# Kernel optimization log

Measured on AMD Instinct MI355X. Metric: run time of the kernel, lower is better.

## Reference

```python
import jax, jax.numpy as jnp
import numpy as np

SPATIAL_SHAPES = ((64, 64), (32, 32), (16, 16), (8, 8))  # (H_l, W_l) per level
N_HEADS, N_LEVELS, N_POINTS = 8, 4, 4
EMBED, HEAD_DIM = 256, 32


def _bilinear_sample(v_lvl, loc, H, W):
    """grid_sample(mode=bilinear, padding=zeros, align_corners=False).

    v_lvl: (B, nH, H*W, d)   loc: (B, Nq, nH, P, 2) with (x, y) in [0, 1].
    Returns (B, nH, Nq, P, d).
    """
    B, nH, _, d = v_lvl.shape
    Nq, P = loc.shape[1], loc.shape[3]
    g = 2.0 * loc - 1.0                      # normalized [-1, 1]
    px = ((g[..., 0] + 1.0) * W - 1.0) * 0.5  # pixel coords, align_corners=False
    py = ((g[..., 1] + 1.0) * H - 1.0) * 0.5
    x0 = jnp.floor(px); y0 = jnp.floor(py)
    wx = px - x0; wy = py - y0
    x0i = x0.astype(jnp.int32); y0i = y0.astype(jnp.int32)
    acc = jnp.zeros((B, nH, Nq * P, d), v_lvl.dtype)
    corners = ((0, 0, (1 - wx) * (1 - wy)), (1, 0, wx * (1 - wy)),
               (0, 1, (1 - wx) * wy), (1, 1, wx * wy))
    for dx, dy, w in corners:
        xi = x0i + dx; yi = y0i + dy
        valid = (xi >= 0) & (xi < W) & (yi >= 0) & (yi < H)
        idx = jnp.clip(yi, 0, H - 1) * W + jnp.clip(xi, 0, W - 1)  # (B,Nq,nH,P)
        idx_t = idx.transpose(0, 2, 1, 3).reshape(B, nH, Nq * P)
        wm = jnp.where(valid, w, 0.0).astype(v_lvl.dtype)
        wm = wm.transpose(0, 2, 1, 3).reshape(B, nH, Nq * P, 1)
        gathered = jnp.take_along_axis(v_lvl, idx_t[..., None], axis=2)
        acc = acc + wm * gathered
    return acc.reshape(B, nH, Nq, P, d)


def setup_inputs() -> dict:
    key = jax.random.key(0)
    ks = jax.random.split(key, 12)
    B, Nq = 4, sum(H * W for H, W in SPATIAL_SHAPES)
    Nv = Nq
    s = 1.0 / np.sqrt(EMBED)
    return {
        "query": jax.random.normal(ks[0], (B, Nq, EMBED), jnp.float32),
        "value": jax.random.normal(ks[1], (B, Nv, EMBED), jnp.float32),
        "reference_points": jax.random.uniform(ks[2], (B, Nq, N_LEVELS, 2), jnp.float32),
        "value_proj_w": jax.random.normal(ks[3], (EMBED, EMBED), jnp.float32) * s,
        "value_proj_b": jnp.zeros((EMBED,), jnp.float32),
        "offsets_w": jax.random.normal(ks[4], (EMBED, N_HEADS * N_LEVELS * N_POINTS * 2), jnp.float32) * (0.05 * s),
        "offsets_b": jax.random.normal(ks[5], (N_HEADS * N_LEVELS * N_POINTS * 2,), jnp.float32) * 2.0,
        "attn_w_w": jax.random.normal(ks[6], (EMBED, N_HEADS * N_LEVELS * N_POINTS), jnp.float32) * s,
        "attn_w_b": jnp.zeros((N_HEADS * N_LEVELS * N_POINTS,), jnp.float32),
        "out_w": jax.random.normal(ks[7], (EMBED, EMBED), jnp.float32) * s,
        "out_b": jnp.zeros((EMBED,), jnp.float32),
    }


def reference(query, value, reference_points, value_proj_w, value_proj_b,
              offsets_w, offsets_b, attn_w_w, attn_w_b, out_w, out_b):
    B, Nq, C = query.shape
    Nv = value.shape[1]
    v = (value @ value_proj_w + value_proj_b).reshape(B, Nv, N_HEADS, HEAD_DIM)
    off = (query @ offsets_w + offsets_b).reshape(B, Nq, N_HEADS, N_LEVELS, N_POINTS, 2)
    aw = (query @ attn_w_w + attn_w_b).reshape(B, Nq, N_HEADS, N_LEVELS * N_POINTS)
    aw = jax.nn.softmax(aw, axis=-1).reshape(B, Nq, N_HEADS, N_LEVELS, N_POINTS)
    norm = jnp.array([[W, H] for H, W in SPATIAL_SHAPES], dtype=query.dtype)  # (L,2) as (W,H)
    loc = reference_points[:, :, None, :, None, :] + off / norm[None, None, None, :, None, :]
    out = jnp.zeros((B, Nq, N_HEADS, HEAD_DIM), query.dtype)
    cursor = 0
    for l, (H, W) in enumerate(SPATIAL_SHAPES):
        v_lvl = v[:, cursor:cursor + H * W].transpose(0, 2, 1, 3)  # (B,nH,HW,d)
        cursor += H * W
        sampled = _bilinear_sample(v_lvl, loc[:, :, :, l], H, W)   # (B,nH,Nq,P,d)
        out = out + jnp.einsum('bnhp,bhnpd->bnhd', aw[:, :, :, l], sampled)
    return out.reshape(B, Nq, C) @ out_w + out_b
```

## Files before the change

### kernel.cpp

```cpp
#include <hip/hip_runtime.h>
#include <hip/hip_bf16.h>
#include <math.h>

#define B_ 4
#define NQ 5440
#define M_ROWS (B_ * NQ)
#define NH 8
#define NL 4
#define NP 4
#define HD 32

typedef __attribute__((ext_vector_type(8))) short bf16x8;
typedef __attribute__((ext_vector_type(4))) short bf16x4;
typedef __attribute__((ext_vector_type(4))) float f32x4;
typedef _Float16 f16;

static __device__ __forceinline__ unsigned short f2bf(float f) {
  union { float f; unsigned u; } v; v.f = f;
  unsigned r = (v.u + 0x7fffu + ((v.u >> 16) & 1u)) >> 16;
  return (unsigned short)r;
}
static __device__ __forceinline__ float bits2f(unsigned u) {
  union { unsigned u; float f; } v; v.u = u; return v.f;
}

__global__ __launch_bounds__(256) void prep_all(
    const float* __restrict__ value, const float* __restrict__ query,
    unsigned short* __restrict__ value_bf, unsigned short* __restrict__ query_bf,
    const float* __restrict__ vpw, const float* __restrict__ offw,
    const float* __restrict__ attnw, const float* __restrict__ outw,
    const float* __restrict__ offb, const float* __restrict__ attnb,
    unsigned short* __restrict__ vp_t, unsigned short* __restrict__ q_t,
    unsigned short* __restrict__ out_t, float* __restrict__ biasq, int n4) {
  int id = blockIdx.x * 256 + threadIdx.x;
  if (id < 2 * n4) {
    const float* src; unsigned short* dst; int j;
    if (id < n4) { src = value; dst = value_bf; j = id; }
    else { src = query; dst = query_bf; j = id - n4; }
    float4 f = ((const float4*)src)[j];
    bf16x4 o;
    o[0] = (short)f2bf(f.x); o[1] = (short)f2bf(f.y);
    o[2] = (short)f2bf(f.z); o[3] = (short)f2bf(f.w);
    ((bf16x4*)dst)[j] = o;
    return;
  }
  int w = id - 2 * n4;
  if (w < 65536) {
    int n = w >> 8, k = w & 255;
    vp_t[w] = f2bf(vpw[k * 256 + n]);
  } else if (w < 163840) {
    int q = w - 65536; int n = q >> 8, k = q & 255;
    q_t[q] = f2bf(n < 256 ? offw[k * 256 + n] : attnw[k * 128 + (n - 256)]);
  } else if (w < 229376) {
    int o = w - 163840; int n = o >> 8, k = o & 255;
    out_t[o] = f2bf(outw[k * 256 + n]);
  } else if (w < 229760) {
    int j = w - 229376;
    biasq[j] = j < 256 ? offb[j] : attnb[j - 256];
  }
}

__global__ __launch_bounds__(256) void gemm12_kernel(
    const unsigned short* __restrict__ valbf, const unsigned short* __restrict__ qrybf,
    const unsigned short* __restrict__ wt_vp, const unsigned short* __restrict__ wt_q,
    const float* __restrict__ vp_b, const float* __restrict__ biasq,
    unsigned short* __restrict__ v_bf, f16* __restrict__ offaw_h) {
  __shared__ unsigned short Bs[8 * 64 * 32];
  const int t = threadIdx.x;
  const int lane = t & 63, wid = t >> 6;
  const int qd = lane >> 4, l16 = lane & 15;
  const int g = blockIdx.x;
  const int grp = g / 80, r = g % 80;
  int by, bx;
  if (grp < 21) { by = grp * 8 + (r & 7); bx = r >> 3; }
  else          { by = 168 + (r & 1);     bx = r >> 1; }
  const int bm = by * 128;
  const bool isv = bx < 4;
  const int bn = isv ? bx * 64 : (bx - 4) * 64;
  const unsigned short* A  = isv ? valbf : qrybf;
  const unsigned short* Wt = isv ? wt_vp : wt_q;

  const unsigned short* bg = Wt + (size_t)(bn + (t >> 2)) * 256 + (t & 3) * 8;
  unsigned short* bs_b = Bs + (t & 192) * 8;
#pragma unroll
  for (int j = 0; j < 8; ++j)
    __builtin_amdgcn_global_load_lds(
        (const __attribute__((address_space(1))) void*)(bg + j * 32),
        (__attribute__((address_space(3))) void*)(bs_b + j * 2048), 16, 0, 0);

  const unsigned short* ar0 = A + (size_t)(bm + wid * 32 + l16) * 256 + qd * 8;
  const unsigned short* ar1 = ar0 + 16 * 256;
  bf16x8 a0[8], a1[8];
#pragma unroll
  for (int j = 0; j < 8; ++j) {
    a0[j] = *(const bf16x8*)(ar0 + j * 32);
    a1[j] = *(const bf16x8*)(ar1 + j * 32);
  }
  __syncthreads();

  f32x4 acc[2][4] = {};
#pragma unroll
  for (int j = 0; j < 8; ++j) {
    const unsigned short* bt = Bs + j * 2048 + l16 * 32 + qd * 8;
#pragma unroll
    for (int ni = 0; ni < 4; ++ni) {
      const bf16x8 bf = *(const bf16x8*)(bt + ni * 512);
      acc[0][ni] = __builtin_amdgcn_mfma_f32_16x16x32_bf16(a0[j], bf, acc[0][ni], 0, 0, 0);
      acc[1][ni] = __builtin_amdgcn_mfma_f32_16x16x32_bf16(a1[j], bf, acc[1][ni], 0, 0, 0);
    }
  }
  if (isv) {
#pragma unroll
    for (int ni = 0; ni < 4; ++ni) {
      const int c = bn + ni * 16 + l16;
      const float bb = vp_b[c];
      const int h = c >> 5, d = c & 31;
#pragma unroll
      for (int mi = 0; mi < 2; ++mi)
#pragma unroll
        for (int rr = 0; rr < 4; ++rr) {
          const int gm = bm + wid * 32 + mi * 16 + qd * 4 + rr;
          const int b = gm / NQ, pix = gm - b * NQ;
          v_bf[((size_t)(b * NH + h) * NQ + pix) * HD + d] = f2bf(acc[mi][ni][rr] + bb);
        }
    }
  } else {
#pragma unroll
    for (int ni = 0; ni < 4; ++ni) {
      const int c = bn + ni * 16 + l16;
      const float bb = biasq[c];
#pragma unroll
      for (int mi = 0; mi < 2; ++mi)
#pragma unroll
        for (int rr = 0; rr < 4; ++rr) {
          const int gm = bm + wid * 32 + mi * 16 + qd * 4 + rr;
          offaw_h[(size_t)gm * 384 + c] = (f16)(acc[mi][ni][rr] + bb);
        }
    }
  }
}

__global__ __launch_bounds__(256) void gemm_out_kernel(
    const unsigned short* __restrict__ attn_bf, const unsigned short* __restrict__ wt_out,
    const float* __restrict__ out_b, float* __restrict__ out) {
  __shared__ unsigned short Bs[8 * 64 * 32];
  const int t = threadIdx.x;
  const int lane = t & 63, wid = t >> 6;
  const int qd = lane >> 4, l16 = lane & 15;
  const int g = blockIdx.x;
  const int grp = g / 32, r = g % 32;
  int by, bx;
  if (grp < 21) { by = grp * 8 + (r & 7); bx = r >> 3; }
  else          { by = 168 + (r & 1);     bx = r >> 1; }
  const int bm = by * 128, bn = bx * 64;

  const unsigned short* bg = wt_out + (size_t)(bn + (t >> 2)) * 256 + (t & 3) * 8;
  unsigned short* bs_b = Bs + (t & 192) * 8;
#pragma unroll
  for (int j = 0; j < 8; ++j)
    __builtin_amdgcn_global_load_lds(
        (const __attribute__((address_space(1))) void*)(bg + j * 32),
        (__attribute__((address_space(3))) void*)(bs_b + j * 2048), 16, 0, 0);

  const unsigned short* ar0 = attn_bf + (size_t)(bm + wid * 32 + l16) * 256 + qd * 8;
  const unsigned short* ar1 = ar0 + 16 * 256;
  bf16x8 a0[8], a1[8];
#pragma unroll
  for (int j = 0; j < 8; ++j) {
    a0[j] = *(const bf16x8*)(ar0 + j * 32);
    a1[j] = *(const bf16x8*)(ar1 + j * 32);
  }
  __syncthreads();

  f32x4 acc[2][4] = {};
#pragma unroll
  for (int j = 0; j < 8; ++j) {
    const unsigned short* bt = Bs + j * 2048 + l16 * 32 + qd * 8;
#pragma unroll
    for (int ni = 0; ni < 4; ++ni) {
      const bf16x8 bf = *(const bf16x8*)(bt + ni * 512);
      acc[0][ni] = __builtin_amdgcn_mfma_f32_16x16x32_bf16(a0[j], bf, acc[0][ni], 0, 0, 0);
      acc[1][ni] = __builtin_amdgcn_mfma_f32_16x16x32_bf16(a1[j], bf, acc[1][ni], 0, 0, 0);
    }
  }
#pragma unroll
  for (int ni = 0; ni < 4; ++ni) {
    const int c = bn + ni * 16 + l16;
    const float bb = out_b[c];
#pragma unroll
    for (int mi = 0; mi < 2; ++mi)
#pragma unroll
      for (int rr = 0; rr < 4; ++rr) {
        const int gm = bm + wid * 32 + mi * 16 + qd * 4 + rr;
        out[(size_t)gm * 256 + c] = acc[mi][ni][rr] + bb;
      }
  }
}

__global__ __launch_bounds__(256) void sample_fused_kernel(
    const unsigned short* __restrict__ v, const float* __restrict__ refp,
    const f16* __restrict__ offaw_h, unsigned short* __restrict__ out) {
  __shared__ float s_off[8 * 384];
  __shared__ float s_ref[64];
  __shared__ unsigned s_offs[16 * 64 * 4];
  __shared__ float s_wts[16 * 64 * 4];
  const int t = threadIdx.x;
  const int blk = blockIdx.x;
  const int b = (blk & 7) >> 1;
  const int q0loc = ((blk >> 3) * 2 + (blk & 1)) * 8;
  const int q0 = b * NQ + q0loc;

  {
    const unsigned* src = (const unsigned*)(offaw_h + (size_t)q0 * 384);
#pragma unroll
    for (int i = 0; i < 6; ++i) {
      const int idx = t + i * 256;
      union { unsigned u; f16 h[2]; } cv; cv.u = src[idx];
      s_off[2 * idx]     = (float)cv.h[0];
      s_off[2 * idx + 1] = (float)cv.h[1];
    }
    if (t < 64) s_ref[t] = refp[(size_t)q0 * 8 + t];
  }
  __syncthreads();
  if (t < 64) {
    float* p = s_off + (t >> 3) * 384 + 256 + (t & 7) * 16;
    float m = -1e30f;
#pragma unroll
    for (int j = 0; j < 16; ++j) m = fmaxf(m, p[j]);
    float e[16]; float s = 0.f;
#pragma unroll
    for (int j = 0; j < 16; ++j) { e[j] = __expf(p[j] - m); s += e[j]; }
    const float inv = 1.f / s;
#pragma unroll
    for (int j = 0; j < 16; ++j) p[j] = e[j] * inv;
  }
  __syncthreads();
  {
    const int qh = t & 63, q = qh >> 3, h = qh & 7, l = t >> 6;
    const int HS[NL]      = {64, 32, 16, 8};
    const int LVL_OFF[NL] = {0, 4096, 5120, 5376};
    const int H = HS[l], W = HS[l];
    const float rx = s_ref[q * 8 + l * 2 + 0];
    const float ry = s_ref[q * 8 + l * 2 + 1];
    const unsigned vbase = (unsigned)(((b * NH + h) * NQ + LVL_OFF[l]) * 64);
#pragma unroll
    for (int pp = 0; pp < 4; ++pp) {
      const int p = l * 4 + pp;
      const float ox = s_off[q * 384 + h * 32 + l * 8 + pp * 2 + 0];
      const float oy = s_off[q * 384 + h * 32 + l * 8 + pp * 2 + 1];
      const float a  = s_off[q * 384 + 256 + h * 16 + p];
      const float px = rx * (float)W + ox - 0.5f;
      const float py = ry * (float)H + oy - 0.5f;
      const float x0f = floorf(px), y0f = floorf(py);
      const int x0 = (int)x0f, y0 = (int)y0f;
      const int x1 = x0 + 1, y1 = y0 + 1;
      const float wx = px - x0f, wy = py - y0f;
      const float m_x0 = (x0 >= 0 && x0 < W) ? 1.f : 0.f;
      const float m_x1 = (x1 >= 0 && x1 < W) ? 1.f : 0.f;
      const float m_y0 = (y0 >= 0 && y0 < H) ? 1.f : 0.f;
      const float m_y1 = (y1 >= 0 && y1 < H) ? 1.f : 0.f;
      const int cx0 = min(max(x0, 0), W - 1), cx1 = min(max(x1, 0), W - 1);
      const int cy0 = min(max(y0, 0), H - 1), cy1 = min(max(y1, 0), H - 1);
      const int ti = (p * 64 + qh) * 4;
      uint4 o4;
      o4.x = vbase + (unsigned)((cy0 * W + cx0) * 64);
      o4.y = vbase + (unsigned)((cy0 * W + cx1) * 64);
      o4.z = vbase + (unsigned)((cy1 * W + cx0) * 64);
      o4.w = vbase + (unsigned)((cy1 * W + cx1) * 64);
      float4 w4;
      w4.x = a * (1.f - wx) * (1.f - wy) * m_x0 * m_y0;
      w4.y = a * wx * (1.f - wy) * m_x1 * m_y0;
      w4.z = a * (1.f - wx) * wy * m_x0 * m_y1;
      w4.w = a * wx * wy * m_x1 * m_y1;
      *(uint4*)&s_offs[ti] = o4;
      *(float4*)&s_wts[ti] = w4;
    }
  }
  __syncthreads();
  const int lane = t & 63, wave = t >> 6;
  const int qloc = wave * 2 + (lane >> 5);
  const int h = (lane >> 2) & 7, d8 = lane & 3;
  const int tqh = qloc * 8 + h;
  const char* vB = (const char*)v;
  const int dof = d8 * 16;
  float acc[8] = {};
#pragma unroll 4
  for (int p = 0; p < 16; ++p) {
    const uint4  o4 = *(const uint4*)&s_offs[(p * 64 + tqh) * 4];
    const float4 w4 = *(const float4*)&s_wts[(p * 64 + tqh) * 4];
    const unsigned off[4] = {o4.x, o4.y, o4.z, o4.w};
    const float wt[4] = {w4.x, w4.y, w4.z, w4.w};
#pragma unroll
    for (int c = 0; c < 4; ++c) {
      union { bf16x8 v8; unsigned u[4]; } cc;
      cc.v8 = *(const bf16x8*)(vB + off[c] + dof);
      const float w = wt[c];
#pragma unroll
      for (int k = 0; k < 4; ++k) {
        acc[2 * k]     += w * bits2f(cc.u[k] << 16);
        acc[2 * k + 1] += w * bits2f(cc.u[k] & 0xffff0000u);
      }
    }
  }
  const int bq = q0 + qloc;
  bf16x8 ov;
#pragma unroll
  for (int k = 0; k < 8; ++k) ov[k] = (short)f2bf(acc[k]);
  *(bf16x8*)(out + (size_t)bq * 256 + h * HD + d8 * 8) = ov;
}

extern "C" void kernel_launch(void* const* d_in, const int* in_sizes, int n_in,
                              void* d_out, int out_size, void* d_ws, size_t ws_size,
                              hipStream_t stream) {
  const float* query        = (const float*)d_in[0];
  const float* value        = (const float*)d_in[1];
  const float* refp         = (const float*)d_in[2];
  const float* value_proj_w = (const float*)d_in[3];
  const float* value_proj_b = (const float*)d_in[4];
  const float* offsets_w    = (const float*)d_in[5];
  const float* offsets_b    = (const float*)d_in[6];
  const float* attn_w_w     = (const float*)d_in[7];
  const float* attn_w_b     = (const float*)d_in[8];
  const float* out_w        = (const float*)d_in[9];
  const float* out_b        = (const float*)d_in[10];
  float* out = (float*)d_out;

  const int M = M_ROWS;
  const size_t SZ_V   = (size_t)M * 256 * 2;
  const size_t SZ_OFF = (size_t)M * 384 * 2;
  char* w = (char*)d_ws;
  unsigned short* value_bf = (unsigned short*)w;
  unsigned short* attn_bf  = (unsigned short*)w;
  unsigned short* query_bf = (unsigned short*)(w + SZ_V);
  unsigned short* v_bf     = (unsigned short*)(w + 2 * SZ_V);
  f16* offaw_h             = (f16*)(w + 3 * SZ_V);
  char* wts                = w + 3 * SZ_V + SZ_OFF;
  unsigned short* wt_vp    = (unsigned short*)wts;
  unsigned short* wt_q     = wt_vp + 65536;
  unsigned short* wt_out   = wt_q + 98304;
  float* biasq             = (float*)(wt_out + 65536);

  dim3 blk(256);
  const int n4 = M * 64;
  const int prep_blocks = (2 * n4 + 229760 + 255) / 256;
  prep_all<<<prep_blocks, blk, 0, stream>>>(
      value, query, value_bf, query_bf,
      value_proj_w, offsets_w, attn_w_w, out_w, offsets_b, attn_w_b,
      wt_vp, wt_q, wt_out, biasq, n4);
  gemm12_kernel<<<1700, blk, 0, stream>>>(
      value_bf, query_bf, wt_vp, wt_q, value_proj_b, biasq, v_bf, offaw_h);
  sample_fused_kernel<<<M / 8, blk, 0, stream>>>(v_bf, refp, offaw_h, attn_bf);
  gemm_out_kernel<<<680, blk, 0, stream>>>(attn_bf, wt_out, out_b, out);
}
```

Before: 173.7 us.

## Compute sampling weights directly from global loads with wave-shuffle softmax

The fused sampling kernel no longer stages the fp16 offsets, logits and reference points through shared memory. Each thread loads its own slice straight from global memory and computes the per-head softmax with xor-shuffles across four lanes, which removes two barriers and a serial softmax stage run by only 64 threads. Corner indices are now stored as 16-bit values, roughly halving the shared-memory index table, and the gather loop is fully unrolled per level with constant level offsets. The cost is more scattered small global loads and some extra address arithmetic in the gather loop.

```diff
diff --git a/kernel.cpp b/kernel.cpp
--- a/kernel.cpp
+++ b/kernel.cpp
@@ -200,10 +200,8 @@
 __global__ __launch_bounds__(256) void sample_fused_kernel(
     const unsigned short* __restrict__ v, const float* __restrict__ refp,
     const f16* __restrict__ offaw_h, unsigned short* __restrict__ out) {
-  __shared__ float s_off[8 * 384];
-  __shared__ float s_ref[64];
-  __shared__ unsigned s_offs[16 * 64 * 4];
-  __shared__ float s_wts[16 * 64 * 4];
+  __shared__ __align__(16) unsigned short s_idx[16 * 64 * 4];
+  __shared__ __align__(16) float s_wts[16 * 64 * 4];
   const int t = threadIdx.x;
   const int blk = blockIdx.x;
   const int b = (blk & 7) >> 1;
@@ -211,68 +209,63 @@
   const int q0 = b * NQ + q0loc;
 
   {
-    const unsigned* src = (const unsigned*)(offaw_h + (size_t)q0 * 384);
-#pragma unroll
-    for (int i = 0; i < 6; ++i) {
-      const int idx = t + i * 256;
-      union { unsigned u; f16 h[2]; } cv; cv.u = src[idx];
-      s_off[2 * idx]     = (float)cv.h[0];
-      s_off[2 * idx + 1] = (float)cv.h[1];
-    }
-    if (t < 64) s_ref[t] = refp[(size_t)q0 * 8 + t];
-  }
-  __syncthreads();
-  if (t < 64) {
-    float* p = s_off + (t >> 3) * 384 + 256 + (t & 7) * 16;
-    float m = -1e30f;
-#pragma unroll
-    for (int j = 0; j < 16; ++j) m = fmaxf(m, p[j]);
-    float e[16]; float s = 0.f;
-#pragma unroll
-    for (int j = 0; j < 16; ++j) { e[j] = __expf(p[j] - m); s += e[j]; }
+    const int lane = t & 63, wave = t >> 6;
+    const int qh = wave * 16 + (lane >> 2);
+    const int l = lane & 3;
+    const int q = qh >> 3, h = qh & 7;
+    const f16* row = offaw_h + (size_t)(q0 + q) * 384;
+    union { uint4 u4; f16 hh[8]; } off8;
+    off8.u4 = *(const uint4*)(row + h * 32 + l * 8);
+    union { uint2 u2; f16 hh[4]; } lg4;
+    lg4.u2 = *(const uint2*)(row + 256 + h * 16 + l * 4);
+    const float2 rxy = *(const float2*)(refp + (size_t)(q0 + q) * 8 + l * 2);
+
+    float lgf[4];
+#pragma unroll
+    for (int j = 0; j < 4; ++j) lgf[j] = (float)lg4.hh[j];
+    float m = fmaxf(fmaxf(lgf[0], lgf[1]), fmaxf(lgf[2], lgf[3]));
+    m = fmaxf(m, __shfl_xor(m, 1));
+    m = fmaxf(m, __shfl_xor(m, 2));
+    float e[4], s = 0.f;
+#pragma unroll
+    for (int j = 0; j < 4; ++j) { e[j] = __expf(lgf[j] - m); s += e[j]; }
+    s += __shfl_xor(s, 1);
+    s += __shfl_xor(s, 2);
     const float inv = 1.f / s;
-#pragma unroll
-    for (int j = 0; j < 16; ++j) p[j] = e[j] * inv;
-  }
-  __syncthreads();
-  {
-    const int qh = t & 63, q = qh >> 3, h = qh & 7, l = t >> 6;
-    const int HS[NL]      = {64, 32, 16, 8};
-    const int LVL_OFF[NL] = {0, 4096, 5120, 5376};
-    const int H = HS[l], W = HS[l];
-    const float rx = s_ref[q * 8 + l * 2 + 0];
-    const float ry = s_ref[q * 8 + l * 2 + 1];
-    const unsigned vbase = (unsigned)(((b * NH + h) * NQ + LVL_OFF[l]) * 64);
+
+    const int Wl = 64 >> l, Hl = 64 >> l;
+    const float pxb = rxy.x * (float)Wl - 0.5f;
+    const float pyb = rxy.y * (float)Hl - 0.5f;
 #pragma unroll
     for (int pp = 0; pp < 4; ++pp) {
       const int p = l * 4 + pp;
-      const float ox = s_off[q * 384 + h * 32 + l * 8 + pp * 2 + 0];
-      const float oy = s_off[q * 384 + h * 32 + l * 8 + pp * 2 + 1];
-      const float a  = s_off[q * 384 + 256 + h * 16 + p];
-      const float px = rx * (float)W + ox - 0.5f;
-      const float py = ry * (float)H + oy - 0.5f;
+      const float ox = (float)off8.hh[pp * 2];
+      const float oy = (float)off8.hh[pp * 2 + 1];
+      const float a  = e[pp] * inv;
+      const float px = pxb + ox;
+      const float py = pyb + oy;
       const float x0f = floorf(px), y0f = floorf(py);
       const int x0 = (int)x0f, y0 = (int)y0f;
       const int x1 = x0 + 1, y1 = y0 + 1;
       const float wx = px - x0f, wy = py - y0f;
-      const float m_x0 = (x0 >= 0 && x0 < W) ? 1.f : 0.f;
-      const float m_x1 = (x1 >= 0 && x1 < W) ? 1.f : 0.f;
-      const float m_y0 = (y0 >= 0 && y0 < H) ? 1.f : 0.f;
-      const float m_y1 = (y1 >= 0 && y1 < H) ? 1.f : 0.f;
-      const int cx0 = min(max(x0, 0), W - 1), cx1 = min(max(x1, 0), W - 1);
-      const int cy0 = min(max(y0, 0), H - 1), cy1 = min(max(y1, 0), H - 1);
+      const float m_x0 = (x0 >= 0 && x0 < Wl) ? 1.f : 0.f;
+      const float m_x1 = (x1 >= 0 && x1 < Wl) ? 1.f : 0.f;
+      const float m_y0 = (y0 >= 0 && y0 < Hl) ? 1.f : 0.f;
+      const float m_y1 = (y1 >= 0 && y1 < Hl) ? 1.f : 0.f;
+      const int cx0 = min(max(x0, 0), Wl - 1), cx1 = min(max(x1, 0), Wl - 1);
+      const int cy0 = min(max(y0, 0), Hl - 1), cy1 = min(max(y1, 0), Hl - 1);
       const int ti = (p * 64 + qh) * 4;
-      uint4 o4;
-      o4.x = vbase + (unsigned)((cy0 * W + cx0) * 64);
-      o4.y = vbase + (unsigned)((cy0 * W + cx1) * 64);
-      o4.z = vbase + (unsigned)((cy1 * W + cx0) * 64);
-      o4.w = vbase + (unsigned)((cy1 * W + cx1) * 64);
+      ushort4 i4;
+      i4.x = (unsigned short)(cy0 * Wl + cx0);
+      i4.y = (unsigned short)(cy0 * Wl + cx1);
+      i4.z = (unsigned short)(cy1 * Wl + cx0);
+      i4.w = (unsigned short)(cy1 * Wl + cx1);
       float4 w4;
       w4.x = a * (1.f - wx) * (1.f - wy) * m_x0 * m_y0;
       w4.y = a * wx * (1.f - wy) * m_x1 * m_y0;
       w4.z = a * (1.f - wx) * wy * m_x0 * m_y1;
       w4.w = a * wx * wy * m_x1 * m_y1;
-      *(uint4*)&s_offs[ti] = o4;
+      *(ushort4*)&s_idx[ti] = i4;
       *(float4*)&s_wts[ti] = w4;
     }
   }
@@ -282,23 +275,31 @@
   const int h = (lane >> 2) & 7, d8 = lane & 3;
   const int tqh = qloc * 8 + h;
   const char* vB = (const char*)v;
-  const int dof = d8 * 16;
+  const unsigned hbase = (unsigned)((b * NH + h) * NQ) * 64u + (unsigned)(d8 * 16);
   float acc[8] = {};
-#pragma unroll 4
-  for (int p = 0; p < 16; ++p) {
-    const uint4  o4 = *(const uint4*)&s_offs[(p * 64 + tqh) * 4];
-    const float4 w4 = *(const float4*)&s_wts[(p * 64 + tqh) * 4];
-    const unsigned off[4] = {o4.x, o4.y, o4.z, o4.w};
-    const float wt[4] = {w4.x, w4.y, w4.z, w4.w};
-#pragma unroll
-    for (int c = 0; c < 4; ++c) {
-      union { bf16x8 v8; unsigned u[4]; } cc;
-      cc.v8 = *(const bf16x8*)(vB + off[c] + dof);
-      const float w = wt[c];
-#pragma unroll
-      for (int k = 0; k < 4; ++k) {
-        acc[2 * k]     += w * bits2f(cc.u[k] << 16);
-        acc[2 * k + 1] += w * bits2f(cc.u[k] & 0xffff0000u);
+#pragma unroll
+  for (int l = 0; l < 4; ++l) {
+    const int LVL_OFF = (l == 0) ? 0 : (l == 1) ? 4096 : (l == 2) ? 5120 : 5376;
+    const unsigned base = hbase + (unsigned)(LVL_OFF * 64);
+#pragma unroll
+    for (int pp = 0; pp < 4; ++pp) {
+      const int p = l * 4 + pp;
+      const ushort4 i4 = *(const ushort4*)&s_idx[(p * 64 + tqh) * 4];
+      const float4 w4 = *(const float4*)&s_wts[(p * 64 + tqh) * 4];
+      const unsigned off[4] = {
+          base + ((unsigned)i4.x << 6), base + ((unsigned)i4.y << 6),
+          base + ((unsigned)i4.z << 6), base + ((unsigned)i4.w << 6)};
+      const float wt[4] = {w4.x, w4.y, w4.z, w4.w};
+#pragma unroll
+      for (int c = 0; c < 4; ++c) {
+        union { bf16x8 v8; unsigned u[4]; } cc;
+        cc.v8 = *(const bf16x8*)(vB + off[c]);
+        const float w = wt[c];
+#pragma unroll
+        for (int k = 0; k < 4; ++k) {
+          acc[2 * k]     += w * bits2f(cc.u[k] << 16);
+          acc[2 * k + 1] += w * bits2f(cc.u[k] & 0xffff0000u);
+        }
       }
     }
   }
```

Measured after the change: 172.2 us. About the same (-0.9%).
